# Performance work log

Measured on AMD Instinct MI355X. Metric: run time of the kernel, lower is better.

The kernel has to match this reference:

```python
import jax, jax.numpy as jnp
import numpy as np

B, L, E, H = 8, 1024, 512, 8
E2 = 2 * E
EPS = 1e-5


def _spectral_fc(x, w, fw, fb, n):
    # rfft along feature dim, multiply by rfft of learned filter w (1,n), irfft back, then Linear
    xf = jnp.fft.rfft(x, axis=2, norm='ortho')          # [B,L,n//2+1] complex
    wf = jnp.fft.rfft(w, axis=1, norm='ortho')          # [1,n//2+1] complex
    y = jnp.fft.irfft(xf * wf, n=n, axis=2, norm='ortho')
    return y @ fw + fb


def _layernorm(x, g, b):
    m = jnp.mean(x, axis=-1, keepdims=True)
    v = jnp.mean(jnp.square(x - m), axis=-1, keepdims=True)
    return (x - m) * jax.lax.rsqrt(v + EPS) * g + b


def setup_inputs() -> dict:
    key = jax.random.key(0)
    ks = jax.random.split(key, 32)
    s = 0.02

    def lin_w(k, i, o):
        return (jax.random.normal(k, (i, o), jnp.float32) / np.sqrt(i)).astype(jnp.float32)

    def layer_params(k0, k1, n):
        return (s * jax.random.normal(k0, (1, n), jnp.float32), lin_w(k1, n, n), jnp.zeros((n,), jnp.float32))

    attn_w, attn_fw, attn_fb = layer_params(ks[1], ks[2], E)
    ln0_w, ln0_fw, ln0_fb = layer_params(ks[3], ks[4], E)
    ln1_w, ln1_fw, ln1_fb = layer_params(ks[5], ks[6], E)
    ln2_w, ln2_fw, ln2_fb = layer_params(ks[7], ks[8], E)
    ln3_w, ln3_fw, ln3_fb = layer_params(ks[9], ks[10], E2)
    ln4_w, ln4_fw, ln4_fb = layer_params(ks[11], ks[12], E2)

    return {
        'x': jax.random.normal(ks[0], (B, L, E), jnp.float32),
        'attn_w': attn_w, 'attn_fw': attn_fw, 'attn_fb': attn_fb,
        'ln0_w': ln0_w, 'ln0_fw': ln0_fw, 'ln0_fb': ln0_fb,
        'ln1_w': ln1_w, 'ln1_fw': ln1_fw, 'ln1_fb': ln1_fb,
        'ln2_w': ln2_w, 'ln2_fw': ln2_fw, 'ln2_fb': ln2_fb,
        'ln3_w': ln3_w, 'ln3_fw': ln3_fw, 'ln3_fb': ln3_fb,
        'ln4_w': ln4_w, 'ln4_fw': ln4_fw, 'ln4_fb': ln4_fb,
        'n1_g': jnp.ones((E,), jnp.float32), 'n1_b': jnp.zeros((E,), jnp.float32),
        'n2_g': jnp.ones((E,), jnp.float32), 'n2_b': jnp.zeros((E,), jnp.float32),
    }


def reference(x, attn_w, attn_fw, attn_fb,
              ln0_w, ln0_fw, ln0_fb, ln1_w, ln1_fw, ln1_fb,
              ln2_w, ln2_fw, ln2_fb, ln3_w, ln3_fw, ln3_fb,
              ln4_w, ln4_fw, ln4_fb, n1_g, n1_b, n2_g, n2_b):
    q = _spectral_fc(x, attn_w, attn_fw, attn_fb, E).reshape(B, L, H, E // H)
    scores = jnp.einsum('blhe,bshe->bhls', q, q) * (1.0 / np.sqrt(E))
    A = jax.nn.softmax(scores, axis=-1)
    new_x = jnp.einsum('bhls,bshd->blhd', A, q).reshape(B, L, E)

    x1 = _layernorm(x + new_x, n1_g, n1_b)
    x_ln = jax.nn.gelu(_spectral_fc(x1, ln0_w, ln0_fw, ln0_fb, E), approximate=False)
    x2 = x1 - x_ln
    h = jax.nn.sigmoid(_spectral_fc(x2, ln1_w, ln1_fw, ln1_fb, E)) * _spectral_fc(x2, ln2_w, ln2_fw, ln2_fb, E)
    out = jnp.concatenate((new_x, x_ln), axis=-1)  # [B,L,2E]
    out = jax.nn.sigmoid(_spectral_fc(out, ln3_w, ln3_fw, ln3_fb, E2)) * _spectral_fc(out, ln4_w, ln4_fw, ln4_fb, E2)
    return (_layernorm(h, n2_g, n2_b), out)
```

## Files before the change

kernel.cpp:

```cpp
#include <hip/hip_runtime.h>
#include <hip/hip_bf16.h>
#include <math.h>

typedef __hip_bfloat16 bf16;
typedef unsigned short u16;
typedef __attribute__((ext_vector_type(8))) short short8;
typedef __attribute__((ext_vector_type(4))) float f32x4;

#define NB      8
#define SEQ     1024
#define EDIM    512
#define E2DIM   1024
#define ROWS    8192
#define INV_SQRT_E 0.04419417382415922f
#define ATT_SCL    0.06375985678148161f

__device__ inline u16 f2bu(float f) {
    union { float f; unsigned u; } c; c.f = f;
    return (u16)((c.u + 0x7FFF + ((c.u >> 16) & 1)) >> 16);
}

__device__ __forceinline__ unsigned cvtpk_bf16(float lo, float hi) {
    unsigned r;
    asm("v_cvt_pk_bf16_f32 %0, %1, %2" : "=v"(r) : "v"(lo), "v"(hi));
    return r;
}

#define VMCNT(N) do { \
    asm volatile("s_waitcnt vmcnt(" #N ")" ::: "memory"); \
    __builtin_amdgcn_sched_barrier(0); \
    __builtin_amdgcn_s_barrier(); \
    __builtin_amdgcn_sched_barrier(0); } while (0)

__device__ __forceinline__ void dma16(const u16* g, u16* l) {
    __builtin_amdgcn_global_load_lds(
        (const __attribute__((address_space(1))) void*)g,
        (__attribute__((address_space(3))) void*)l, 16, 0, 0);
}

__global__ __launch_bounds__(256) void detect_dtype(const u16* __restrict__ x,
                                                    int* __restrict__ flag) {
    int t = threadIdx.x;
    int cnt = 0;
    for (int k = t; k < 8192; k += 256) {
        int e = (x[k] >> 7) & 0xFF;
        if (e >= 0xC0) cnt++;
    }
#pragma unroll
    for (int o = 32; o > 0; o >>= 1) cnt += __shfl_xor(cnt, o);
    __shared__ int red[4];
    if ((t & 63) == 0) red[t >> 6] = cnt;
    __syncthreads();
    if (t == 0) flag[0] = (red[0] + red[1] + red[2] + red[3] > 100) ? 1 : 0;
}

struct CvtBatch {
    const void* src[23];
    float4*     dst[23];
    int         pre4[24];
};

__global__ __launch_bounds__(256) void cvt_all(CvtBatch a, int total4,
                                               const int* __restrict__ flag) {
    int t = blockIdx.x * 256 + threadIdx.x;
    if (t >= total4) return;
    int lo = 0;
    while (t >= a.pre4[lo + 1]) lo++;
    int li = t - a.pre4[lo];
    if (flag[0]) {
        a.dst[lo][li] = ((const float4*)a.src[lo])[li];
    } else {
        ushort4 u = ((const ushort4*)a.src[lo])[li];
        union { unsigned int i; float f; } c;
        float4 o;
        c.i = ((unsigned)u.x) << 16; o.x = c.f;
        c.i = ((unsigned)u.y) << 16; o.y = c.f;
        c.i = ((unsigned)u.z) << 16; o.z = c.f;
        c.i = ((unsigned)u.w) << 16; o.w = c.f;
        a.dst[lo][li] = o;
    }
}

__global__ __launch_bounds__(256) void f2b_kernel(const float* __restrict__ src,
                                                  u16* __restrict__ dst, int n4) {
    int i = blockIdx.x * 256 + threadIdx.x;
    if (i >= n4) return;
    float4 a = ((const float4*)src)[i];
    ushort4 o;
    o.x = f2bu(a.x); o.y = f2bu(a.y); o.z = f2bu(a.z); o.w = f2bu(a.w);
    ((ushort4*)dst)[i] = o;
}

#define LDK 32

__device__ __forceinline__ void stage64x64sw(const u16* g0, int ld, u16* lds,
                                             int wave, int lane) {
#pragma unroll
    for (int c = 0; c < 2; c++) {
        const int r  = wave * 16 + c * 8 + (lane >> 3);
        const int cg = (lane & 7) ^ (r & 7);
        const u16* g = g0 + (size_t)r * ld + cg * 8;
        u16* l = lds + (wave * 16 + c * 8) * 64;
        dma16(g, l);
    }
}

__device__ __forceinline__ void xcd_swz(int& bx, int& by) {
    const int nx  = gridDim.x;
    const int nwg = nx * gridDim.y;
    const int lid = blockIdx.y * nx + blockIdx.x;
    const int q   = nwg >> 3;
    const int s   = (lid & 7) * q + (lid >> 3);
    bx = s % nx;
    by = s / nx;
}

struct FoldBatch {
    const float* w[6];
    const float* fw[6];
    u16* t1[6];
    u16* t2[6];
    u16* mt[6];
    int  n[6], lg[6];
    float sc[6];
};

__global__ __launch_bounds__(256) void fold_trconv(FoldBatch fb) {
    const int z = blockIdx.z;
    const int n = fb.n[z];
    const int bx = blockIdx.x * 32, by = blockIdx.y * 32;
    if (bx >= n || by >= n) return;
    __shared__ float t[32][33];
    const int tx = threadIdx.x & 31, ty = threadIdx.x >> 5;
    const float* src = fb.fw[z];
    u16* dst = fb.t1[z];
#pragma unroll
    for (int r = 0; r < 32; r += 8)
        t[ty + r][tx] = src[(size_t)(by + ty + r) * n + bx + tx];
    __syncthreads();
#pragma unroll
    for (int r = 0; r < 32; r += 8)
        dst[(size_t)(bx + ty + r) * n + by + tx] = f2bu(t[tx][ty + r]);
}

__global__ __launch_bounds__(256) void fold_circ(FoldBatch fb) {
    const int z = blockIdx.z;
    const int n = fb.n[z], lg = fb.lg[z];
    int idx = blockIdx.x * 256 + threadIdx.x;
    if (idx >= n * n) return;
    int mask = n - 1;
    int m = idx & mask;
    int j = idx >> lg;
    fb.t2[z][idx] = f2bu(fb.w[z][(m - j) & mask]);
}

__global__ __launch_bounds__(256) void fold_gemm(FoldBatch fb) {
    const int z = blockIdx.z;
    const int n = fb.n[z];
    const int bm = blockIdx.y * 128, bn = blockIdx.x * 128;
    if (bm >= n || bn >= n) return;
    const u16* A  = fb.t1[z];
    const u16* Bt = fb.t2[z];
    u16* Mt = fb.mt[z];
    const float scale = fb.sc[z];

    __shared__ u16 Asl[3][128 * LDK];
    __shared__ u16 Bsl[3][128 * LDK];
    const int tid = threadIdx.x;
    const int lane = tid & 63, wave = tid >> 6;
    const int wy = wave >> 1, wx = wave & 1;
    const int qd = lane >> 4, ln16 = lane & 15;
    const int ca = (qd ^ ((ln16 >> 1) & 3)) * 8;

    const int srow = wave * 16 + (lane >> 2);
    const int scol = ((lane & 3) ^ ((lane >> 3) & 3)) * 8;
    const int lo   = wave * 16 * LDK;
    const size_t a64 = (size_t)64 * n;
    const u16* pA = A  + (size_t)bm * n + (size_t)srow * n + scol;
    const u16* pB = Bt + (size_t)bn * n + (size_t)srow * n + scol;

    f32x4 acc[4][4];
#pragma unroll
    for (int i = 0; i < 4; i++)
#pragma unroll
        for (int j = 0; j < 4; j++)
#pragma unroll
            for (int r = 0; r < 4; r++) acc[i][j][r] = 0.f;

#define STAGE_FG(bi) do { \
    dma16(pA,       &Asl[bi][lo]); \
    dma16(pA + a64, &Asl[bi][lo + 64 * LDK]); \
    dma16(pB,       &Bsl[bi][lo]); \
    dma16(pB + a64, &Bsl[bi][lo + 64 * LDK]); \
    pA += 32; pB += 32; } while (0)

    const int nt = n >> 5;
    STAGE_FG(0);
    STAGE_FG(1);
    int cur = 0, stg = 2;
    for (int t = 0; t < nt; ++t) {
        if (t < nt - 1) { VMCNT(4); } else { VMCNT(0); }
        const u16* Ac = Asl[cur];
        const u16* Bc = Bsl[cur];
        short8 af[4], bf_[4];
#pragma unroll
        for (int i = 0; i < 4; i++) {
            af[i]  = *(const short8*)&Ac[(wy * 64 + i * 16 + ln16) * LDK + ca];
            bf_[i] = *(const short8*)&Bc[(wx * 64 + i * 16 + ln16) * LDK + ca];
        }
        if (t + 2 < nt) STAGE_FG(stg);
#pragma unroll
        for (int i = 0; i < 4; i++)
#pragma unroll
            for (int j = 0; j < 4; j++)
                acc[i][j] = __builtin_amdgcn_mfma_f32_16x16x32_bf16(af[i], bf_[j], acc[i][j], 0, 0, 0);
        cur = (cur == 2) ? 0 : cur + 1;
        stg = (stg == 2) ? 0 : stg + 1;
    }
#undef STAGE_FG
#pragma unroll
    for (int i = 0; i < 4; i++)
#pragma unroll
        for (int j = 0; j < 4; j++) {
            const int col = bn + wx * 64 + j * 16 + ln16;
#pragma unroll
            for (int r = 0; r < 4; r++) {
                const int row = bm + wy * 64 + i * 16 + qd * 4 + r;
                Mt[(size_t)row * n + col] = f2bu(acc[i][j][r] * scale);
            }
        }
}

__global__ __launch_bounds__(256) void gemm_bf(
    const u16* __restrict__ A, int lda,
    const u16* __restrict__ Bt, int ldb,
    const float* __restrict__ bias,
    float* __restrict__ Cf, int ldc,
    u16* __restrict__ Cb, int ldcb,
    u16* __restrict__ Cb2, int ldcb2,
    const float* __restrict__ aux, int ldaux,
    int K, int mode)
{
    __shared__ u16 Asl[3][128 * LDK];
    __shared__ u16 Bsl[3][64 * LDK];
    const int tid = threadIdx.x;
    int bxs, bys;
    xcd_swz(bxs, bys);
    const int bm = bys * 128, bn = bxs * 64;
    const int lane = tid & 63, wave = tid >> 6;
    const int wy = wave >> 1, wx = wave & 1;
    const int qd = lane >> 4, ln16 = lane & 15;
    const int ca = (qd ^ ((ln16 >> 1) & 3)) * 8;

    const int srow = wave * 16 + (lane >> 2);
    const int scol = ((lane & 3) ^ ((lane >> 3) & 3)) * 8;
    const int lo   = wave * 16 * LDK;
    const size_t a64 = (size_t)64 * lda;
    const u16* pA = A  + (size_t)bm * lda + (size_t)srow * lda + scol;
    const u16* pB = Bt + (size_t)bn * ldb + (size_t)srow * ldb + scol;

    f32x4 acc[4][2];
#pragma unroll
    for (int i = 0; i < 4; i++)
#pragma unroll
        for (int j = 0; j < 2; j++)
#pragma unroll
            for (int r = 0; r < 4; r++) acc[i][j][r] = 0.f;

#define STAGE_GB(bi) do { \
    dma16(pA,       &Asl[bi][lo]); \
    dma16(pA + a64, &Asl[bi][lo + 64 * LDK]); \
    dma16(pB,       &Bsl[bi][lo]); \
    pA += 32; pB += 32; } while (0)

    const int nt = K >> 5;
    STAGE_GB(0);
    STAGE_GB(1);
    int cur = 0, stg = 2;
    for (int t = 0; t < nt; ++t) {
        if (t < nt - 1) { VMCNT(3); } else { VMCNT(0); }
        const u16* Ac = Asl[cur];
        const u16* Bc = Bsl[cur];
        short8 af[4], bf_[2];
#pragma unroll
        for (int i = 0; i < 4; i++)
            af[i]  = *(const short8*)&Ac[(wy * 64 + i * 16 + ln16) * LDK + ca];
#pragma unroll
        for (int j = 0; j < 2; j++)
            bf_[j] = *(const short8*)&Bc[(wx * 32 + j * 16 + ln16) * LDK + ca];
        if (t + 2 < nt) STAGE_GB(stg);
#pragma unroll
        for (int i = 0; i < 4; i++)
#pragma unroll
            for (int j = 0; j < 2; j++)
                acc[i][j] = __builtin_amdgcn_mfma_f32_16x16x32_bf16(af[i], bf_[j], acc[i][j], 0, 0, 0);
        cur = (cur == 2) ? 0 : cur + 1;
        stg = (stg == 2) ? 0 : stg + 1;
    }
#undef STAGE_GB

#pragma unroll
    for (int i = 0; i < 4; i++) {
#pragma unroll
        for (int j = 0; j < 2; j++) {
            const int col = bn + wx * 32 + j * 16 + ln16;
            const float b_ = bias ? bias[col] : 0.f;
#pragma unroll
            for (int r = 0; r < 4; r++) {
                const int row = bm + wy * 64 + i * 16 + qd * 4 + r;
                float v = acc[i][j][r] + b_;
                if (mode == 1) v = 0.5f * v * (1.0f + erff(v * 0.7071067811865476f));
                if (Cf)  Cf[(size_t)row * ldc + col] = v;
                if (Cb)  Cb[(size_t)row * ldcb + col] = f2bu(v);
                if (Cb2) Cb2[(size_t)row * ldcb2 + col] =
                             f2bu(aux[(size_t)row * ldaux + col] - v);
            }
        }
    }
}

__global__ __launch_bounds__(256) void gemm_bf2(
    const u16* __restrict__ A, int lda,
    const u16* __restrict__ B1t, const u16* __restrict__ B2t, int ldb,
    const float* __restrict__ bias1, const float* __restrict__ bias2,
    float* __restrict__ Cf, int ldc, int K)
{
    __shared__ u16 Asl[3][128 * LDK];
    __shared__ u16 B1sl[3][64 * LDK];
    __shared__ u16 B2sl[3][64 * LDK];
    const int tid = threadIdx.x;
    int bxs, bys;
    xcd_swz(bxs, bys);
    const int bm = bys * 128, bn = bxs * 64;
    const int lane = tid & 63, wave = tid >> 6;
    const int wy = wave >> 1, wx = wave & 1;
    const int qd = lane >> 4, ln16 = lane & 15;
    const int ca = (qd ^ ((ln16 >> 1) & 3)) * 8;

    const int srow = wave * 16 + (lane >> 2);
    const int scol = ((lane & 3) ^ ((lane >> 3) & 3)) * 8;
    const int lo   = wave * 16 * LDK;
    const size_t a64 = (size_t)64 * lda;
    const u16* pA  = A   + (size_t)bm * lda + (size_t)srow * lda + scol;
    const u16* pB1 = B1t + (size_t)bn * ldb + (size_t)srow * ldb + scol;
    const u16* pB2 = B2t + (size_t)bn * ldb + (size_t)srow * ldb + scol;

    f32x4 acc1[4][2], acc2[4][2];
#pragma unroll
    for (int i = 0; i < 4; i++)
#pragma unroll
        for (int j = 0; j < 2; j++)
#pragma unroll
            for (int r = 0; r < 4; r++) { acc1[i][j][r] = 0.f; acc2[i][j][r] = 0.f; }

#define STAGE_GB2(bi) do { \
    dma16(pA,       &Asl[bi][lo]); \
    dma16(pA + a64, &Asl[bi][lo + 64 * LDK]); \
    dma16(pB1,      &B1sl[bi][lo]); \
    dma16(pB2,      &B2sl[bi][lo]); \
    pA += 32; pB1 += 32; pB2 += 32; } while (0)

    const int nt = K >> 5;
    STAGE_GB2(0);
    STAGE_GB2(1);
    int cur = 0, stg = 2;
    for (int t = 0; t < nt; ++t) {
        if (t < nt - 1) { VMCNT(4); } else { VMCNT(0); }
        const u16* Ac  = Asl[cur];
        const u16* B1c = B1sl[cur];
        const u16* B2c = B2sl[cur];
        short8 af[4], b1f[2], b2f[2];
#pragma unroll
        for (int i = 0; i < 4; i++)
            af[i]  = *(const short8*)&Ac [(wy * 64 + i * 16 + ln16) * LDK + ca];
#pragma unroll
        for (int j = 0; j < 2; j++) {
            b1f[j] = *(const short8*)&B1c[(wx * 32 + j * 16 + ln16) * LDK + ca];
            b2f[j] = *(const short8*)&B2c[(wx * 32 + j * 16 + ln16) * LDK + ca];
        }
        if (t + 2 < nt) STAGE_GB2(stg);
#pragma unroll
        for (int i = 0; i < 4; i++)
#pragma unroll
            for (int j = 0; j < 2; j++) {
                acc1[i][j] = __builtin_amdgcn_mfma_f32_16x16x32_bf16(af[i], b1f[j], acc1[i][j], 0, 0, 0);
                acc2[i][j] = __builtin_amdgcn_mfma_f32_16x16x32_bf16(af[i], b2f[j], acc2[i][j], 0, 0, 0);
            }
        cur = (cur == 2) ? 0 : cur + 1;
        stg = (stg == 2) ? 0 : stg + 1;
    }
#undef STAGE_GB2

#pragma unroll
    for (int i = 0; i < 4; i++) {
#pragma unroll
        for (int j = 0; j < 2; j++) {
            const int col = bn + wx * 32 + j * 16 + ln16;
            const float b1_ = bias1[col], b2_ = bias2[col];
#pragma unroll
            for (int r = 0; r < 4; r++) {
                const int row = bm + wy * 64 + i * 16 + qd * 4 + r;
                const float g = 1.0f / (1.0f + expf(-(acc1[i][j][r] + b1_)));
                Cf[(size_t)row * ldc + col] = g * (acc2[i][j][r] + b2_);
            }
        }
    }
}

__global__ __launch_bounds__(256) void ln_kernel(
    const float* __restrict__ in0, int ld0,
    const u16* __restrict__ in1b, int ld1b,
    const float* __restrict__ g, const float* __restrict__ bta,
    float* __restrict__ outf, int ldo,
    u16* __restrict__ outb, int ldob)
{
    int row = blockIdx.x, tid = threadIdx.x;
    const float* p0 = in0 + (size_t)row * ld0;
    float v0 = p0[tid], v1 = p0[tid + 256];
    if (in1b) {
        const u16* p1 = in1b + (size_t)row * ld1b;
        union { unsigned u; float f; } c0, c1;
        c0.u = ((unsigned)p1[tid]) << 16;
        c1.u = ((unsigned)p1[tid + 256]) << 16;
        v0 += c0.f; v1 += c1.f;
    }
    float s = v0 + v1, sq = v0 * v0 + v1 * v1;
#pragma unroll
    for (int o = 32; o > 0; o >>= 1) {
        s  += __shfl_xor(s, o);
        sq += __shfl_xor(sq, o);
    }
    __shared__ float red[8];
    int wid = tid >> 6;
    if ((tid & 63) == 0) { red[wid] = s; red[4 + wid] = sq; }
    __syncthreads();
    s  = red[0] + red[1] + red[2] + red[3];
    sq = red[4] + red[5] + red[6] + red[7];
    float mean = s * (1.0f / 512.0f);
    float var  = sq * (1.0f / 512.0f) - mean * mean;
    float rstd = rsqrtf(var + 1e-5f);
    float o0 = (v0 - mean) * rstd * g[tid] + bta[tid];
    float o1 = (v1 - mean) * rstd * g[tid + 256] + bta[tid + 256];
    if (outf) {
        outf[(size_t)row * ldo + tid]       = o0;
        outf[(size_t)row * ldo + tid + 256] = o1;
    }
    if (outb) {
        outb[(size_t)row * ldob + tid]       = f2bu(o0);
        outb[(size_t)row * ldob + tid + 256] = f2bu(o1);
    }
}

__global__ __launch_bounds__(256) void trans_vt(const u16* __restrict__ q,
                                                u16* __restrict__ vt) {
    const int z  = blockIdx.z;
    const int bb = z >> 3, hh = z & 7;
    const int k0 = blockIdx.x * 64;
    const int d0 = blockIdx.y * 32;
    __shared__ u16 t[64][33];
    const int tx = threadIdx.x & 31, ty = threadIdx.x >> 5;
    const u16* src = q + (size_t)(bb * SEQ + k0) * EDIM + hh * 64 + d0;
#pragma unroll
    for (int r = 0; r < 64; r += 8)
        t[ty + r][tx] = src[(size_t)(ty + r) * EDIM + tx];
    __syncthreads();
    const int ox = threadIdx.x & 63, oy = threadIdx.x >> 6;
    u16* dst = vt + ((size_t)z * 64 + d0) * SEQ + k0;
#pragma unroll
    for (int r = 0; r < 32; r += 4)
        dst[(size_t)(oy + r) * SEQ + ox] = t[ox][oy + r];
}

#define AP 80
#define ANT 16

__global__ __launch_bounds__(256) void attn_mfma(const u16* __restrict__ qall,
                                                 const u16* __restrict__ vt,
                                                 u16* __restrict__ catb) {
    __shared__ u16 Ks[64 * 64];
    __shared__ u16 VTs[64 * 64];
    __shared__ u16 Pw[4][16 * AP];

    const int phys = blockIdx.x;
    const int bid = (phys & 7) * 128 + (phys >> 3);
    const int lt = bid & 15, hh = (bid >> 4) & 7, bb = bid >> 7;
    const int q0 = lt * 64;
    const int tid = threadIdx.x;
    const int wave = tid >> 6, lane = tid & 63;
    const int quad = lane >> 4, ln16 = lane & 15;

    const u16* qh = qall + (size_t)bb * SEQ * EDIM + hh * 64;
    const u16* vh = vt + (size_t)(bb * 8 + hh) * 64 * SEQ;

    const u16* qrow = qh + (size_t)(q0 + wave * 16 + ln16) * EDIM + quad * 8;
    const short8 aq0 = *(const short8*)(qrow);
    const short8 aq1 = *(const short8*)(qrow + 32);

    f32x4 oacc[4];
    float m_run = -1e30f, l_run = 0.f;
#pragma unroll
    for (int j = 0; j < 4; j++)
#pragma unroll
        for (int r = 0; r < 4; r++) oacc[j][r] = 0.f;

    const int sw = ln16 & 7;
    const int c0 = (quad ^ sw) * 8;
    const int c1 = ((quad + 4) ^ sw) * 8;

    for (int t = 0; t < ANT; ++t) {
        if (t) __syncthreads();
        stage64x64sw(qh + (size_t)t * 64 * EDIM, EDIM, Ks, wave, lane);
        stage64x64sw(vh + t * 64, SEQ, VTs, wave, lane);
        __syncthreads();

        f32x4 S[4];
#pragma unroll
        for (int j = 0; j < 4; j++) {
            const int ro = (j * 16 + ln16) * 64;
            short8 a0 = *(const short8*)&Ks[ro + c0];
            short8 a1 = *(const short8*)&Ks[ro + c1];
            f32x4 c = {0.f, 0.f, 0.f, 0.f};
            c = __builtin_amdgcn_mfma_f32_16x16x32_bf16(a0, aq0, c, 0, 0, 0);
            c = __builtin_amdgcn_mfma_f32_16x16x32_bf16(a1, aq1, c, 0, 0, 0);
            S[j] = c;
        }

        float mx = S[0][0];
#pragma unroll
        for (int j = 0; j < 4; j++)
#pragma unroll
            for (int r = 0; r < 4; r++) mx = fmaxf(mx, S[j][r]);
        mx = fmaxf(mx, __shfl_xor(mx, 16));
        mx = fmaxf(mx, __shfl_xor(mx, 32));
        const float mn = fmaxf(m_run, mx);
        const float al = exp2f((m_run - mn) * ATT_SCL);
        m_run = mn;
        const float ns = -mn * ATT_SCL;
        float p[4][4];
        float rs = 0.f;
#pragma unroll
        for (int j = 0; j < 4; j++)
#pragma unroll
            for (int r = 0; r < 4; r++) {
                p[j][r] = exp2f(fmaf(S[j][r], ATT_SCL, ns));
                rs += p[j][r];
            }
        rs += __shfl_xor(rs, 16);
        rs += __shfl_xor(rs, 32);
        l_run = l_run * al + rs;

#pragma unroll
        for (int j = 0; j < 4; j++) {
            unsigned w0 = cvtpk_bf16(p[j][0], p[j][1]);
            unsigned w1 = cvtpk_bf16(p[j][2], p[j][3]);
            *(uint2*)&Pw[wave][ln16 * AP + j * 16 + quad * 4] = make_uint2(w0, w1);
        }

        float alq[4];
#pragma unroll
        for (int r = 0; r < 4; r++) alq[r] = __shfl(al, quad * 4 + r);
#pragma unroll
        for (int j = 0; j < 4; j++)
#pragma unroll
            for (int r = 0; r < 4; r++) oacc[j][r] *= alq[r];

        short8 pa0 = *(const short8*)&Pw[wave][ln16 * AP + quad * 8];
        short8 pa1 = *(const short8*)&Pw[wave][ln16 * AP + 32 + quad * 8];
#pragma unroll
        for (int j = 0; j < 4; j++) {
            const int ro = (j * 16 + ln16) * 64;
            short8 b0 = *(const short8*)&VTs[ro + c0];
            short8 b1 = *(const short8*)&VTs[ro + c1];
            oacc[j] = __builtin_amdgcn_mfma_f32_16x16x32_bf16(pa0, b0, oacc[j], 0, 0, 0);
            oacc[j] = __builtin_amdgcn_mfma_f32_16x16x32_bf16(pa1, b1, oacc[j], 0, 0, 0);
        }
    }

    const float linv = 1.0f / l_run;
    float invq[4];
#pragma unroll
    for (int r = 0; r < 4; r++) invq[r] = __shfl(linv, quad * 4 + r);
#pragma unroll
    for (int r = 0; r < 4; r++) {
        const int row = bb * SEQ + q0 + wave * 16 + quad * 4 + r;
#pragma unroll
        for (int j = 0; j < 4; j++) {
            const int col = hh * 64 + j * 16 + ln16;
            catb[(size_t)row * E2DIM + col] = f2bu(oacc[j][r] * invq[r]);
        }
    }
}

extern "C" void kernel_launch(void* const* d_in, const int* in_sizes, int n_in,
                              void* d_out, int out_size, void* d_ws, size_t ws_size,
                              hipStream_t stream)
{
    const size_t OFF_MT0 = 0;
    const size_t OFF_MT1 = OFF_MT0 + 131072;
    const size_t OFF_MT2 = OFF_MT1 + 131072;
    const size_t OFF_MT3 = OFF_MT2 + 131072;
    const size_t OFF_MT4 = OFF_MT3 + 131072;
    const size_t OFF_MT5 = OFF_MT4 + 524288;
    const size_t OFF_XB  = OFF_MT5 + 524288;
    const size_t OFF_CB  = OFF_XB + 2097152;
    const size_t OFF_BQ  = OFF_CB + 4194304;
    const size_t OFF_BN  = OFF_BQ + 4194304;
    const size_t OFF_BC  = OFF_BN + 4194304;
    const size_t OFF_P   = OFF_BC + 4194304;

    float* W = (float*)d_ws;
    u16* MT[6] = {(u16*)(W + OFF_MT0), (u16*)(W + OFF_MT1), (u16*)(W + OFF_MT2),
                  (u16*)(W + OFF_MT3), (u16*)(W + OFF_MT4), (u16*)(W + OFF_MT5)};
    u16*   XB  = (u16*)(W + OFF_XB);
    u16*   CB  = (u16*)(W + OFF_CB);
    u16*   QB  = (u16*)(W + OFF_BQ);
    float* BN  = W + OFF_BN;
    float* BC  = W + OFF_BC;
    u16*   VT  = (u16*)BN;

    float* F[23];
    CvtBatch cb;
    int pre = 0;
    for (int i = 0; i < 23 && i < n_in; i++) {
        cb.pre4[i] = pre;
        F[i] = W + OFF_P + (size_t)pre * 4;
        cb.src[i] = d_in[i];
        cb.dst[i] = (float4*)F[i];
        pre += in_sizes[i] / 4;
    }
    cb.pre4[23] = pre;
    const int total4 = pre;
    int* FLAG = (int*)(W + OFF_P + (size_t)total4 * 4);

    if (n_in < 23) return;
    if (ws_size < (OFF_P + (size_t)total4 * 4 + 16) * sizeof(float)) return;

    detect_dtype<<<1, 256, 0, stream>>>((const u16*)d_in[0], FLAG);
    cvt_all<<<(total4 + 255) / 256, 256, 0, stream>>>(cb, total4, FLAG);
    f2b_kernel<<<(ROWS * EDIM / 4 + 255) / 256, 256, 0, stream>>>(F[0], XB, ROWS * EDIM / 4);

    FoldBatch fb;
    {
        const int wi[6] = {1, 4, 7, 10, 13, 16};
        u16* T1 = (u16*)BN;
        u16* T2 = (u16*)BC;
        size_t off = 0;
        for (int s = 0; s < 6; s++) {
            const int n = (s < 4) ? 512 : 1024;
            fb.w[s]  = F[wi[s]];
            fb.fw[s] = F[wi[s] + 1];
            fb.t1[s] = T1 + off;
            fb.t2[s] = T2 + off;
            fb.mt[s] = MT[s];
            fb.n[s]  = n;
            fb.lg[s] = (s < 4) ? 9 : 10;
            fb.sc[s] = (s < 4) ? 0.04419417382415922f : 0.03125f;
            off += (size_t)n * n;
        }
    }
    fold_trconv<<<dim3(32, 32, 6), 256, 0, stream>>>(fb);
    fold_circ<<<dim3(4096, 1, 6), 256, 0, stream>>>(fb);
    fold_gemm<<<dim3(8, 8, 6), 256, 0, stream>>>(fb);

    float* out0 = (float*)d_out;
    float* out1 = (float*)d_out + (size_t)ROWS * EDIM;

    gemm_bf<<<dim3(8, 64), 256, 0, stream>>>(
        XB, 512, MT[0], 512, F[3], nullptr, 0, QB, 512, nullptr, 0, nullptr, 0, 512, 0);
    trans_vt<<<dim3(16, 2, 64), 256, 0, stream>>>(QB, VT);
    attn_mfma<<<1024, 256, 0, stream>>>(QB, VT, CB);
    ln_kernel<<<8192, 256, 0, stream>>>(F[0], 512, CB, 1024, F[19], F[20],
                                        BC, 512, XB, 512);
    gemm_bf<<<dim3(8, 64), 256, 0, stream>>>(
        XB, 512, MT[1], 512, F[6], nullptr, 0, CB + 512, 1024, QB, 512, BC, 512, 512, 1);
    gemm_bf2<<<dim3(8, 64), 256, 0, stream>>>(
        QB, 512, MT[2], MT[3], 512, F[9], F[12], BN, 512, 512);
    ln_kernel<<<8192, 256, 0, stream>>>(BN, 512, nullptr, 0, F[21], F[22],
                                        out0, 512, nullptr, 0);
    gemm_bf2<<<dim3(16, 64), 256, 0, stream>>>(
        CB, 1024, MT[4], MT[5], 1024, F[15], F[18], out1, 1024, 1024);
}
```

Measured before the change: 331.4 us.

## Double-buffer K/V tiles in attention kernel and skip redundant rescale

The attention kernel now keeps two LDS buffers for the K and V^T tiles. It prefetches tile t+2 with async global-to-LDS loads while computing on tile t, using vmcnt waits in place of full syncthreads around each staging step. V fragments are read into registers before the barrier so the buffer can be refilled early. The online-softmax accumulator rescale is skipped when no row max changed in the wave. This doubles the LDS used for K/V, which may lower occupancy, and adds a divergent branch.

```diff
diff --git a/kernel.cpp b/kernel.cpp
--- a/kernel.cpp
+++ b/kernel.cpp
@@ -28,6 +28,12 @@
 
 #define VMCNT(N) do { \
     asm volatile("s_waitcnt vmcnt(" #N ")" ::: "memory"); \
+    __builtin_amdgcn_sched_barrier(0); \
+    __builtin_amdgcn_s_barrier(); \
+    __builtin_amdgcn_sched_barrier(0); } while (0)
+
+#define LGKM0_BAR() do { \
+    asm volatile("s_waitcnt lgkmcnt(0)" ::: "memory"); \
     __builtin_amdgcn_sched_barrier(0); \
     __builtin_amdgcn_s_barrier(); \
     __builtin_amdgcn_sched_barrier(0); } while (0)
@@ -92,18 +98,6 @@
 }
 
 #define LDK 32
-
-__device__ __forceinline__ void stage64x64sw(const u16* g0, int ld, u16* lds,
-                                             int wave, int lane) {
-#pragma unroll
-    for (int c = 0; c < 2; c++) {
-        const int r  = wave * 16 + c * 8 + (lane >> 3);
-        const int cg = (lane & 7) ^ (r & 7);
-        const u16* g = g0 + (size_t)r * ld + cg * 8;
-        u16* l = lds + (wave * 16 + c * 8) * 64;
-        dma16(g, l);
-    }
-}
 
 __device__ __forceinline__ void xcd_swz(int& bx, int& by) {
     const int nx  = gridDim.x;
@@ -477,8 +471,8 @@
 __global__ __launch_bounds__(256) void attn_mfma(const u16* __restrict__ qall,
                                                  const u16* __restrict__ vt,
                                                  u16* __restrict__ catb) {
-    __shared__ u16 Ks[64 * 64];
-    __shared__ u16 VTs[64 * 64];
+    __shared__ u16 Ks[2][64 * 64];
+    __shared__ u16 VTs[2][64 * 64];
     __shared__ u16 Pw[4][16 * AP];
 
     const int phys = blockIdx.x;
@@ -507,18 +501,37 @@
     const int c0 = (quad ^ sw) * 8;
     const int c1 = ((quad + 4) ^ sw) * 8;
 
+    const int r0  = wave * 16 + (lane >> 3);
+    const int r1  = r0 + 8;
+    const int cg0 = (lane & 7) ^ (r0 & 7);
+    const int cg1 = (lane & 7) ^ (r1 & 7);
+    const u16* pK0 = qh + (size_t)r0 * EDIM + cg0 * 8;
+    const u16* pK1 = qh + (size_t)r1 * EDIM + cg1 * 8;
+    const u16* pV0 = vh + (size_t)r0 * SEQ + cg0 * 8;
+    const u16* pV1 = vh + (size_t)r1 * SEQ + cg1 * 8;
+    const int lds0 = (wave * 16) * 64;
+    const int lds1 = (wave * 16 + 8) * 64;
+
+#define ASTAGE(bi, t) do { \
+    dma16(pK0 + (size_t)(t) * 64 * EDIM, &Ks[bi][lds0]); \
+    dma16(pK1 + (size_t)(t) * 64 * EDIM, &Ks[bi][lds1]); \
+    dma16(pV0 + (t) * 64, &VTs[bi][lds0]); \
+    dma16(pV1 + (t) * 64, &VTs[bi][lds1]); } while (0)
+
+    ASTAGE(0, 0);
+    ASTAGE(1, 1);
+    int cur = 0;
     for (int t = 0; t < ANT; ++t) {
-        if (t) __syncthreads();
-        stage64x64sw(qh + (size_t)t * 64 * EDIM, EDIM, Ks, wave, lane);
-        stage64x64sw(vh + t * 64, SEQ, VTs, wave, lane);
-        __syncthreads();
+        if (t < ANT - 1) { VMCNT(4); } else { VMCNT(0); }
+        const u16* Kc = Ks[cur];
+        const u16* Vc = VTs[cur];
 
         f32x4 S[4];
 #pragma unroll
         for (int j = 0; j < 4; j++) {
             const int ro = (j * 16 + ln16) * 64;
-            short8 a0 = *(const short8*)&Ks[ro + c0];
-            short8 a1 = *(const short8*)&Ks[ro + c1];
+            short8 a0 = *(const short8*)&Kc[ro + c0];
+            short8 a1 = *(const short8*)&Kc[ro + c1];
             f32x4 c = {0.f, 0.f, 0.f, 0.f};
             c = __builtin_amdgcn_mfma_f32_16x16x32_bf16(a0, aq0, c, 0, 0, 0);
             c = __builtin_amdgcn_mfma_f32_16x16x32_bf16(a1, aq1, c, 0, 0, 0);
@@ -532,8 +545,11 @@
             for (int r = 0; r < 4; r++) mx = fmaxf(mx, S[j][r]);
         mx = fmaxf(mx, __shfl_xor(mx, 16));
         mx = fmaxf(mx, __shfl_xor(mx, 32));
+        const float m_old = m_run;
         const float mn = fmaxf(m_run, mx);
-        const float al = exp2f((m_run - mn) * ATT_SCL);
+        const bool anynew = __any(mx > m_old);
+        float al = 1.0f;
+        if (anynew) al = exp2f((m_old - mn) * ATT_SCL);
         m_run = mn;
         const float ns = -mn * ATT_SCL;
         float p[4][4];
@@ -556,25 +572,37 @@
             *(uint2*)&Pw[wave][ln16 * AP + j * 16 + quad * 4] = make_uint2(w0, w1);
         }
 
-        float alq[4];
-#pragma unroll
-        for (int r = 0; r < 4; r++) alq[r] = __shfl(al, quad * 4 + r);
-#pragma unroll
-        for (int j = 0; j < 4; j++)
-#pragma unroll
-            for (int r = 0; r < 4; r++) oacc[j][r] *= alq[r];
-
         short8 pa0 = *(const short8*)&Pw[wave][ln16 * AP + quad * 8];
         short8 pa1 = *(const short8*)&Pw[wave][ln16 * AP + 32 + quad * 8];
+        short8 vb0[4], vb1[4];
 #pragma unroll
         for (int j = 0; j < 4; j++) {
             const int ro = (j * 16 + ln16) * 64;
-            short8 b0 = *(const short8*)&VTs[ro + c0];
-            short8 b1 = *(const short8*)&VTs[ro + c1];
-            oacc[j] = __builtin_amdgcn_mfma_f32_16x16x32_bf16(pa0, b0, oacc[j], 0, 0, 0);
-            oacc[j] = __builtin_amdgcn_mfma_f32_16x16x32_bf16(pa1, b1, oacc[j], 0, 0, 0);
-        }
-    }
+            vb0[j] = *(const short8*)&Vc[ro + c0];
+            vb1[j] = *(const short8*)&Vc[ro + c1];
+        }
+
+        LGKM0_BAR();
+        if (t + 2 < ANT) ASTAGE(cur, t + 2);
+
+        if (anynew) {
+            float alq[4];
+#pragma unroll
+            for (int r = 0; r < 4; r++) alq[r] = __shfl(al, quad * 4 + r);
+#pragma unroll
+            for (int j = 0; j < 4; j++)
+#pragma unroll
+                for (int r = 0; r < 4; r++) oacc[j][r] *= alq[r];
+        }
+
+#pragma unroll
+        for (int j = 0; j < 4; j++) {
+            oacc[j] = __builtin_amdgcn_mfma_f32_16x16x32_bf16(pa0, vb0[j], oacc[j], 0, 0, 0);
+            oacc[j] = __builtin_amdgcn_mfma_f32_16x16x32_bf16(pa1, vb1[j], oacc[j], 0, 0, 0);
+        }
+        cur ^= 1;
+    }
+#undef ASTAGE
 
     const float linv = 1.0f / l_run;
     float invq[4];
```

Result: no change. 332.6 us (+0.4%).
